# Performance work log

Hardware: AMD Instinct MI355X
Metric: run time of the kernel (lower is better)

The kernel has to match this reference:

```python
import jax, jax.numpy as jnp
import numpy as np
from jax import lax

B, W, H, C = 32, 512, 512, 3
PSF = 32


def setup_inputs() -> dict:
    key = jax.random.key(0)
    k1, k2, k3 = jax.random.split(key, 3)
    observed_images = jax.random.normal(k1, (B, W, H, C), dtype=jnp.float32)
    # trainable vars of the keras model (estimated_image would be initialized to
    # mean(observed) on the first call; we treat it as a free parameter)
    estimated_image = jax.random.normal(k2, (W, H, C), dtype=jnp.float32)
    point_spread_functions = jax.random.normal(k3, (B, PSF, PSF, 1, C), dtype=jnp.float32) * 0.05
    return {
        "observed_images": observed_images,
        "estimated_image": estimated_image,
        "point_spread_functions": point_spread_functions,
    }


def _per_example_conv(img_nhwc, psf_hwio):
    # img_nhwc: [1, W, H, C]; psf_hwio: [k, k, 1, C] -> grouped (depthwise) conv,
    # feature_group_count = C, matching tf.nn.conv2d's grouped-conv semantics.
    out = lax.conv_general_dilated(
        img_nhwc, psf_hwio,
        window_strides=(1, 1), padding="SAME",
        dimension_numbers=("NHWC", "HWIO", "NHWC"),
        feature_group_count=img_nhwc.shape[-1],
    )
    return out[0]  # [W, H, C]


def reference(observed_images, estimated_image, point_spread_functions):
    img = estimated_image[None]  # [1, W, H, C], shared across batch
    # vmap over the per-example PSF kernels replaces the python loop of B conv2d calls
    predicted = jax.vmap(lambda psf: _per_example_conv(img, psf))(point_spread_functions)
    # predicted: [B, W, H, C]
    loss = jnp.mean((observed_images - predicted) ** 2)
    return predicted, loss
```

## Files before the change

kernel.cpp:

```cpp
#include <hip/hip_runtime.h>
#include <hip/hip_bf16.h>

#define BATCH 32
#define WDIM 512
#define HDIM 512
#define CDIM 3
#define KPSF 32
#define NPRED (BATCH*WDIM*HDIM*CDIM)

#define TW 88
#define TH 63
#define TE (TW*TH)
#define TALL (TW*TH*CDIM)

typedef __bf16 bf16x8 __attribute__((ext_vector_type(8)));
typedef float floatx16 __attribute__((ext_vector_type(16)));
typedef float fx4 __attribute__((ext_vector_type(4)));

__device__ __forceinline__ void barrier_lgkm() {
    __asm__ volatile("s_waitcnt lgkmcnt(0)\n\ts_barrier" ::: "memory");
}

__global__ __launch_bounds__(64) void pack_psf(const float* __restrict__ psf,
                                               __bf16* __restrict__ dst,
                                               float* __restrict__ loss) {
    if (blockIdx.x == 0 && threadIdx.x == 0) *loss = 0.f;
    int idx = blockIdx.x;
    int h = idx & 1;
    int j = (idx >> 1) & 31;
    int c = idx >> 6;
    int lane = threadIdx.x;
    int b = lane & 31;
    int q = lane >> 5;
    bf16x8 v;
#pragma unroll
    for (int t = 0; t < 8; ++t) {
        int i = 16*h + 8*q + t;
        v[t] = (__bf16)psf[((size_t)(b*KPSF + i)*KPSF + j)*CDIM + c];
    }
    *(bf16x8*)(dst + (size_t)(idx*64 + lane)*8) = v;
}

__global__ __launch_bounds__(384, 3) void conv_mfma(
    const float* __restrict__ obs,
    const float* __restrict__ img,
    const __bf16* __restrict__ psfA,
    float* __restrict__ out)
{
    __shared__ __align__(16) unsigned char smem[CDIM*TE*2];
    __bf16 (*sImg)[TE] = (__bf16 (*)[TE])smem;
    float* sOut = (float*)smem;

    const int tid  = threadIdx.x;
    const int lane = tid & 63;
    const int w    = tid >> 6;
    const int c    = w >> 1;
    const int h    = w & 1;
    const int n    = lane & 31;
    const int q    = lane >> 5;

    const int bx = blockIdx.x;
    const int r8 = bx & 7;
    const int g  = (bx >> 3) & 7;
    const int yt = bx >> 6;
    const int x0 = g*64 + r8;
    const int ytile = yt*32;

    const bool interior = (x0 >= 15) && (x0 <= WDIM - 73) &&
                          (ytile >= 15) && (ytile <= HDIM - 48);
    if (interior) {
        const int col0 = (ytile - 15)*3;
        const int p2 = col0 & 3;
        const float* gb = img + (size_t)(x0 - 15)*(HDIM*CDIM) + (col0 - p2);
#pragma unroll 2
        for (int f = tid; f < 88*48; f += 384) {
            int r = f / 48;
            int v = f - r*48;
            fx4 val = *(const fx4*)(gb + (size_t)r*(HDIM*CDIM) + 4*v);
            int d = 4*v - p2;
#pragma unroll
            for (int u = 0; u < 4; ++u) {
                int dd = d + u;
                if (dd >= 0 && dd < 189) {
                    int yl = (dd*171) >> 9;
                    int cc = dd - 3*yl;
                    sImg[cc][yl*TW + r] = (__bf16)val[u];
                }
            }
        }
    } else {
#pragma unroll 4
        for (int e = tid; e < TALL; e += 384) {
            int xl = e / (TH*CDIM);
            int rr = e - xl*(TH*CDIM);
            int yl = rr / 3;
            int cc = rr - yl*3;
            int xg = x0 + xl - 15;
            int yg = ytile + yl - 15;
            float v = 0.f;
            if ((unsigned)xg < WDIM && (unsigned)yg < HDIM)
                v = img[((size_t)xg*HDIM + yg)*CDIM + cc];
            sImg[cc][yl*TW + xl] = (__bf16)v;
        }
    }
    __syncthreads();

    floatx16 acc[4] = {};
    const __bf16* pA = psfA + (size_t)c*(KPSF*2*64*8) + (size_t)lane*8;
    const __bf16* sI = (const __bf16*)&sImg[c][q*8 + h*32];

    bf16x8 A0 = *(const bf16x8*)(pA);
    bf16x8 A1 = *(const bf16x8*)(pA + 512);
#pragma unroll 2
    for (int j = 0; j < 32; ++j) {
        bf16x8 cA0 = A0, cA1 = A1;
        if (j < 31) {
            A0 = *(const bf16x8*)(pA + (size_t)(j+1)*1024);
            A1 = *(const bf16x8*)(pA + (size_t)(j+1)*1024 + 512);
        }
        const __bf16* rowp = sI + (n + j)*TW;
        bf16x8 C[6];
#pragma unroll
        for (int rr = 0; rr < 6; ++rr)
            C[rr] = *(const bf16x8*)(rowp + rr*8);
#pragma unroll
        for (int s = 0; s < 4; ++s) {
            acc[s] = __builtin_amdgcn_mfma_f32_32x32x16_bf16(cA0, C[s],   acc[s], 0, 0, 0);
            acc[s] = __builtin_amdgcn_mfma_f32_32x32x16_bf16(cA1, C[s+2], acc[s], 0, 0, 0);
        }
    }

    float ls = 0.f;
    size_t base[4];
#pragma unroll
    for (int k = 0; k < 4; ++k) {
        int f = tid + 384*k;
        int sl = f / 768;
        int g2 = f - sl*768;
        int fb = g2 / 24;
        int r4 = (g2 - fb*24) * 4;
        base[k] = (((size_t)fb*WDIM + x0 + 32*sl)*HDIM + ytile)*CDIM + r4;
    }
    fx4 obA[4], obB[4];
#pragma unroll
    for (int k = 0; k < 4; ++k)
        obA[k] = __builtin_nontemporal_load((const fx4*)&obs[base[k]]);
#pragma unroll
    for (int k = 0; k < 4; ++k)
        obB[k] = __builtin_nontemporal_load((const fx4*)&obs[base[k] + 8*HDIM*CDIM]);

#pragma unroll
    for (int t = 0; t < 4; ++t) {
        barrier_lgkm();
#pragma unroll
        for (int rr = 0; rr < 16; ++rr) {
            int b = (rr & 3) + 8*(rr >> 2) + 4*q;
            sOut[h*3072 + (b*32 + n)*3 + c] = acc[t][rr];
        }
        barrier_lgkm();
        fx4 cur[4];
#pragma unroll
        for (int k = 0; k < 4; ++k) { cur[k] = obA[k]; obA[k] = obB[k]; }
        if (t < 2) {
#pragma unroll
            for (int k = 0; k < 4; ++k)
                obB[k] = __builtin_nontemporal_load(
                    (const fx4*)&obs[base[k] + (size_t)(t+2)*8*HDIM*CDIM]);
        }
#pragma unroll
        for (int k = 0; k < 4; ++k) {
            fx4 p = *(const fx4*)&sOut[4*(tid + 384*k)];
            __builtin_nontemporal_store(p, (fx4*)&out[base[k] + (size_t)t*8*HDIM*CDIM]);
            fx4 d = cur[k] - p;
            ls += d[0]*d[0] + d[1]*d[1] + d[2]*d[2] + d[3]*d[3];
        }
    }

#pragma unroll
    for (int m = 32; m >= 1; m >>= 1) ls += __shfl_xor(ls, m, 64);
    if (lane == 0) atomicAdd(out + NPRED, ls * (1.0f/(float)NPRED));
}

extern "C" void kernel_launch(void* const* d_in, const int* in_sizes, int n_in,
                              void* d_out, int out_size, void* d_ws, size_t ws_size,
                              hipStream_t stream) {
    const float* obs = (const float*)d_in[0];
    const float* img = (const float*)d_in[1];
    const float* psf = (const float*)d_in[2];
    float* out = (float*)d_out;
    __bf16* psfA = (__bf16*)d_ws;

    pack_psf<<<192, 64, 0, stream>>>(psf, psfA, out + NPRED);
    conv_mfma<<<1024, 384, 0, stream>>>(obs, img, psfA, out);
}
```

Measured before the change: 261.8 us.

## Process two y-tiles per block with double-buffered LDS and 32-bit offsets

Each block now handles two y-tiles sequentially, so the grid is halved. The second tile is staged into a separate LDS region after the first tile's epilogue, and its observation loads are issued before its MMA loop. This amortizes per-block setup and lets tile staging overlap other waves' work. Address arithmetic is switched from size_t to unsigned to cut 64-bit integer ops. The cost is a larger LDS footprint (about 57 KB), which may cut blocks per CU and with it occupancy, and half as many blocks to spread across CUs.

Result: slower. 315.3 us (+20.4%).

```diff
diff --git a/kernel.cpp b/kernel.cpp
--- a/kernel.cpp
+++ b/kernel.cpp
@@ -12,6 +12,9 @@
 #define TH 63
 #define TE (TW*TH)
 #define TALL (TW*TH*CDIM)
+
+#define SIMG_B_OFF 24576
+#define LDS_BYTES 57856
 
 typedef __bf16 bf16x8 __attribute__((ext_vector_type(8)));
 typedef float floatx16 __attribute__((ext_vector_type(16)));
@@ -41,31 +44,9 @@
     *(bf16x8*)(dst + (size_t)(idx*64 + lane)*8) = v;
 }
 
-__global__ __launch_bounds__(384, 3) void conv_mfma(
-    const float* __restrict__ obs,
-    const float* __restrict__ img,
-    const __bf16* __restrict__ psfA,
-    float* __restrict__ out)
-{
-    __shared__ __align__(16) unsigned char smem[CDIM*TE*2];
-    __bf16 (*sImg)[TE] = (__bf16 (*)[TE])smem;
-    float* sOut = (float*)smem;
-
-    const int tid  = threadIdx.x;
-    const int lane = tid & 63;
-    const int w    = tid >> 6;
-    const int c    = w >> 1;
-    const int h    = w & 1;
-    const int n    = lane & 31;
-    const int q    = lane >> 5;
-
-    const int bx = blockIdx.x;
-    const int r8 = bx & 7;
-    const int g  = (bx >> 3) & 7;
-    const int yt = bx >> 6;
-    const int x0 = g*64 + r8;
-    const int ytile = yt*32;
-
+__device__ __forceinline__ void stage_tile(__bf16* sImg ,
+                                           const float* __restrict__ img,
+                                           int tid, int x0, int ytile) {
     const bool interior = (x0 >= 15) && (x0 <= WDIM - 73) &&
                           (ytile >= 15) && (ytile <= HDIM - 48);
     if (interior) {
@@ -84,7 +65,7 @@
                 if (dd >= 0 && dd < 189) {
                     int yl = (dd*171) >> 9;
                     int cc = dd - 3*yl;
-                    sImg[cc][yl*TW + r] = (__bf16)val[u];
+                    sImg[cc*TE + yl*TW + r] = (__bf16)val[u];
                 }
             }
         }
@@ -100,15 +81,14 @@
             float v = 0.f;
             if ((unsigned)xg < WDIM && (unsigned)yg < HDIM)
                 v = img[((size_t)xg*HDIM + yg)*CDIM + cc];
-            sImg[cc][yl*TW + xl] = (__bf16)v;
-        }
-    }
-    __syncthreads();
-
-    floatx16 acc[4] = {};
-    const __bf16* pA = psfA + (size_t)c*(KPSF*2*64*8) + (size_t)lane*8;
-    const __bf16* sI = (const __bf16*)&sImg[c][q*8 + h*32];
-
+            sImg[cc*TE + yl*TW + xl] = (__bf16)v;
+        }
+    }
+}
+
+__device__ __forceinline__ void main_loop(floatx16 acc[4],
+                                          const __bf16* __restrict__ pA,
+                                          const __bf16* sIc, int n) {
     bf16x8 A0 = *(const bf16x8*)(pA);
     bf16x8 A1 = *(const bf16x8*)(pA + 512);
 #pragma unroll 2
@@ -118,7 +98,7 @@
             A0 = *(const bf16x8*)(pA + (size_t)(j+1)*1024);
             A1 = *(const bf16x8*)(pA + (size_t)(j+1)*1024 + 512);
         }
-        const __bf16* rowp = sI + (n + j)*TW;
+        const __bf16* rowp = sIc + (n + j)*TW;
         bf16x8 C[6];
 #pragma unroll
         for (int rr = 0; rr < 6; ++rr)
@@ -129,9 +109,9 @@
             acc[s] = __builtin_amdgcn_mfma_f32_32x32x16_bf16(cA1, C[s+2], acc[s], 0, 0, 0);
         }
     }
-
-    float ls = 0.f;
-    size_t base[4];
+}
+
+__device__ __forceinline__ void compute_bases(unsigned base[4], int tid, int x0, int ytile) {
 #pragma unroll
     for (int k = 0; k < 4; ++k) {
         int f = tid + 384*k;
@@ -139,16 +119,20 @@
         int g2 = f - sl*768;
         int fb = g2 / 24;
         int r4 = (g2 - fb*24) * 4;
-        base[k] = (((size_t)fb*WDIM + x0 + 32*sl)*HDIM + ytile)*CDIM + r4;
-    }
-    fx4 obA[4], obB[4];
-#pragma unroll
-    for (int k = 0; k < 4; ++k)
-        obA[k] = __builtin_nontemporal_load((const fx4*)&obs[base[k]]);
+        base[k] = ((unsigned)(fb*WDIM + x0 + 32*sl)*HDIM + (unsigned)ytile)*CDIM + r4;
+    }
+}
+
+__device__ __forceinline__ void epilogue(const floatx16 acc[4], float* sOut,
+                                         const unsigned base[4], fx4 obA[4],
+                                         const float* __restrict__ obs,
+                                         float* __restrict__ out,
+                                         int tid, int n, int q, int c, int h,
+                                         float& ls) {
+    fx4 obB[4];
 #pragma unroll
     for (int k = 0; k < 4; ++k)
         obB[k] = __builtin_nontemporal_load((const fx4*)&obs[base[k] + 8*HDIM*CDIM]);
-
 #pragma unroll
     for (int t = 0; t < 4; ++t) {
         barrier_lgkm();
@@ -165,16 +149,78 @@
 #pragma unroll
             for (int k = 0; k < 4; ++k)
                 obB[k] = __builtin_nontemporal_load(
-                    (const fx4*)&obs[base[k] + (size_t)(t+2)*8*HDIM*CDIM]);
+                    (const fx4*)&obs[base[k] + (unsigned)(t+2)*8*HDIM*CDIM]);
         }
 #pragma unroll
         for (int k = 0; k < 4; ++k) {
             fx4 p = *(const fx4*)&sOut[4*(tid + 384*k)];
-            __builtin_nontemporal_store(p, (fx4*)&out[base[k] + (size_t)t*8*HDIM*CDIM]);
+            __builtin_nontemporal_store(p, (fx4*)&out[base[k] + (unsigned)t*8*HDIM*CDIM]);
             fx4 d = cur[k] - p;
             ls += d[0]*d[0] + d[1]*d[1] + d[2]*d[2] + d[3]*d[3];
         }
     }
+}
+
+__global__ __launch_bounds__(384, 3) void conv_mfma(
+    const float* __restrict__ obs,
+    const float* __restrict__ img,
+    const __bf16* __restrict__ psfA,
+    float* __restrict__ out)
+{
+    __shared__ __align__(16) unsigned char smem[LDS_BYTES];
+    __bf16* sImgA = (__bf16*)smem;
+    __bf16* sImgB = (__bf16*)(smem + SIMG_B_OFF);
+    float*  sOutA = (float*)smem;
+    float*  sOutB = (float*)(smem + SIMG_B_OFF);
+
+    const int tid  = threadIdx.x;
+    const int lane = tid & 63;
+    const int w    = tid >> 6;
+    const int c    = w >> 1;
+    const int h    = w & 1;
+    const int n    = lane & 31;
+    const int q    = lane >> 5;
+
+    const int bx = blockIdx.x;
+    const int r8 = bx & 7;
+    const int g  = (bx >> 3) & 7;
+    const int z  = bx >> 6;
+    const int x0 = g*64 + r8;
+    const int yt1 = z*32;
+    const int yt2 = (z + 8)*32;
+
+    const __bf16* pA = psfA + (size_t)c*(KPSF*2*64*8) + (size_t)lane*8;
+
+    stage_tile(sImgA, img, tid, x0, yt1);
+    __syncthreads();
+
+    unsigned base1[4];
+    compute_bases(base1, tid, x0, yt1);
+    fx4 obA[4];
+#pragma unroll
+    for (int k = 0; k < 4; ++k)
+        obA[k] = __builtin_nontemporal_load((const fx4*)&obs[base1[k]]);
+
+    floatx16 acc1[4] = {};
+    main_loop(acc1, pA, sImgA + c*TE + q*8 + h*32, n);
+
+    float ls = 0.f;
+    epilogue(acc1, sOutA, base1, obA, obs, out, tid, n, q, c, h, ls);
+
+    stage_tile(sImgB, img, tid, x0, yt2);
+
+    unsigned base2[4];
+    compute_bases(base2, tid, x0, yt2);
+#pragma unroll
+    for (int k = 0; k < 4; ++k)
+        obA[k] = __builtin_nontemporal_load((const fx4*)&obs[base2[k]]);
+
+    barrier_lgkm();
+
+    floatx16 acc2[4] = {};
+    main_loop(acc2, pA, sImgB + c*TE + q*8 + h*32, n);
+
+    epilogue(acc2, sOutB, base2, obA, obs, out, tid, n, q, c, h, ls);
 
 #pragma unroll
     for (int m = 32; m >= 1; m >>= 1) ls += __shfl_xor(ls, m, 64);
@@ -191,5 +237,5 @@
     __bf16* psfA = (__bf16*)d_ws;
 
     pack_psf<<<192, 64, 0, stream>>>(psf, psfA, out + NPRED);
-    conv_mfma<<<1024, 384, 0, stream>>>(obs, img, psfA, out);
-}
+    conv_mfma<<<512, 384, 0, stream>>>(obs, img, psfA, out);
+}
```
